# Performance work log

Measured on AMD Instinct MI355X. Metric: run time of the kernel, lower is better.

## Reference

```python
import jax, jax.numpy as jnp
import numpy as np

FEATURE_SIZE = 1000000  # padding index == FEATURE_SIZE
NEG_INF = -1e9


def _attn_pool(emb_table, hist_idx, ad_idx):
    # hist_idx: [B, L] int, ad_idx: [B] int
    hist = emb_table[hist_idx]          # [B, L, K] gather
    ad = emb_table[ad_idx]              # [B, K]
    score = jnp.einsum('blk,bk->bl', hist, ad)          # [B, L]
    score = jnp.where(hist_idx != FEATURE_SIZE, score, NEG_INF)
    w = jax.nn.softmax(score, axis=1)
    return jnp.einsum('blk,bl->bk', hist, w)            # [B, K]


def setup_inputs() -> dict:
    key = jax.random.key(0)
    ks = jax.random.split(key, 12)
    B, F, K = 4096, 8, 64
    V = FEATURE_SIZE + 1
    d_in = 3 * K + F * K  # 704
    inp = {
        'feature_idx': jax.random.randint(ks[0], (B, F), 0, FEATURE_SIZE),
        'hist_item': jax.random.randint(ks[1], (B, 350), 0, V),
        'hist_author': jax.random.randint(ks[2], (B, 250), 0, V),
        'hist_music': jax.random.randint(ks[3], (B, 100), 0, V),
        'emb_table': jax.random.normal(ks[4], (V, K), jnp.float32),
        'W1': jax.random.normal(ks[5], (d_in, 512), jnp.float32) * 0.02,
        'b1': jnp.zeros((512,), jnp.float32),
        'W2': jax.random.normal(ks[6], (512, 256), jnp.float32) * 0.02,
        'b2': jnp.zeros((256,), jnp.float32),
        'W3': jax.random.normal(ks[7], (256, 128), jnp.float32) * 0.02,
        'b3': jnp.zeros((128,), jnp.float32),
        'Wo': jax.random.normal(ks[8], (128, 1), jnp.float32) * 0.02,
        'bo': jnp.zeros((1,), jnp.float32),
    }
    return inp


def reference(feature_idx, hist_item, hist_author, hist_music, emb_table,
              W1, b1, W2, b2, W3, b3, Wo, bo):
    # ad indices for the three behavior features: columns 2, 3, 6
    pools = [
        _attn_pool(emb_table, hist_item, feature_idx[:, 2]),
        _attn_pool(emb_table, hist_author, feature_idx[:, 3]),
        _attn_pool(emb_table, hist_music, feature_idx[:, 6]),
    ]
    user_beha = jnp.concatenate(pools, axis=1)                    # [B, 3K]
    B = feature_idx.shape[0]
    ad_emb = emb_table[feature_idx].reshape(B, -1)                # [B, F*K]
    x = jnp.concatenate([user_beha, ad_emb], axis=1)              # [B, 704]
    x = jax.nn.relu(x @ W1 + b1)
    x = jax.nn.relu(x @ W2 + b2)
    x = jax.nn.relu(x @ W3 + b3)
    logits = x @ Wo + bo                                          # [B, 1]
    return logits
```

## Files before the change

### kernel.cpp

```cpp
#include <hip/hip_runtime.h>
#include <cstddef>

#define BATCH   4096
#define PAD_IDX 1000000
#define NEG_INF_F (-1e9f)

typedef __attribute__((ext_vector_type(8))) short bf16x8;
typedef __attribute__((ext_vector_type(4))) float f32x4;
typedef unsigned short u16;

__device__ __forceinline__ u16 f2bf(float f) {
    unsigned u = __float_as_uint(f);
    return (u16)((u + 0x7fffu + ((u >> 16) & 1u)) >> 16);
}
__device__ __forceinline__ float bf2f(u16 b) {
    return __uint_as_float(((unsigned)b) << 16);
}


#define UPD(s, v)                                     \
    {                                                 \
        float nm = fmaxf(m, (s));                     \
        float sc = __expf(m - nm);                    \
        float e  = __expf((s) - nm);                  \
        d = fmaf(d, sc, e);                           \
        acc.x = fmaf(acc.x, sc, e * (v).x);           \
        acc.y = fmaf(acc.y, sc, e * (v).y);           \
        acc.z = fmaf(acc.z, sc, e * (v).z);           \
        acc.w = fmaf(acc.w, sc, e * (v).w);           \
        m = nm;                                       \
    }

#define MERGE(P)                                                  \
    {                                                             \
        float mo  = __shfl_xor(m, P);                             \
        float d_o = __shfl_xor(d, P);                             \
        float ax = __shfl_xor(acc.x, P);                          \
        float ay = __shfl_xor(acc.y, P);                          \
        float az = __shfl_xor(acc.z, P);                          \
        float aw = __shfl_xor(acc.w, P);                          \
        float nm = fmaxf(m, mo);                                  \
        float sA = __expf(m - nm), sB = __expf(mo - nm);          \
        d = d * sA + d_o * sB;                                    \
        acc.x = acc.x * sA + ax * sB;                             \
        acc.y = acc.y * sA + ay * sB;                             \
        acc.z = acc.z * sA + az * sB;                             \
        acc.w = acc.w * sA + aw * sB;                             \
        m = nm;                                                   \
    }

#define QRED(s)                       \
    s += __shfl_xor(s, 1);            \
    s += __shfl_xor(s, 2);            \
    s += __shfl_xor(s, 4);            \
    s += __shfl_xor(s, 8);

__global__ void __launch_bounds__(256) build_x_kernel(
    const int* __restrict__ fidx,
    const int* __restrict__ hist_item,
    const int* __restrict__ hist_author,
    const int* __restrict__ hist_music,
    const float* __restrict__ emb,
    u16* __restrict__ x)
{
    const int w    = (blockIdx.x * 256 + threadIdx.x) >> 6;
    const int lane = threadIdx.x & 63;
    const int t16  = lane & 15;
    const int q    = lane >> 4;

    if (w < 3 * BATCH) {
        const int h = w >> 12;
        const int b = w & (BATCH - 1);
        int L, col, off;
        const int* hrow;
        if (h == 0)      { L = 350; col = 2; off = 0;   hrow = hist_item   + (size_t)b * 350; }
        else if (h == 1) { L = 250; col = 3; off = 64;  hrow = hist_author + (size_t)b * 250; }
        else             { L = 100; col = 6; off = 128; hrow = hist_music  + (size_t)b * 100; }

        const int ad_idx = fidx[b * 8 + col];
        const float4 ad4 = *(const float4*)(emb + (size_t)ad_idx * 64 + 4 * t16);

        float m = NEG_INF_F, d = 0.f;
        float4 acc = make_float4(0.f, 0.f, 0.f, 0.f);

        int l = 0;
        for (; l + 8 <= L; l += 8) {
            const int i0 = hrow[l + q];
            const int i1 = hrow[l + 4 + q];
            const float4 v0 = *(const float4*)(emb + (size_t)i0 * 64 + 4 * t16);
            const float4 v1 = *(const float4*)(emb + (size_t)i1 * 64 + 4 * t16);
            float s0 = v0.x * ad4.x + v0.y * ad4.y + v0.z * ad4.z + v0.w * ad4.w;
            float s1 = v1.x * ad4.x + v1.y * ad4.y + v1.z * ad4.z + v1.w * ad4.w;
            QRED(s0)
            QRED(s1)
            if (i0 == PAD_IDX) s0 = NEG_INF_F;
            if (i1 == PAD_IDX) s1 = NEG_INF_F;
            UPD(s0, v0)
            UPD(s1, v1)
        }
        for (; l < L; l += 4) {
            const int li = l + q;
            const int i0 = (li < L) ? hrow[li] : PAD_IDX;
            const float4 v0 = *(const float4*)(emb + (size_t)i0 * 64 + 4 * t16);
            float s0 = v0.x * ad4.x + v0.y * ad4.y + v0.z * ad4.z + v0.w * ad4.w;
            QRED(s0)
            if (i0 == PAD_IDX) s0 = NEG_INF_F;
            UPD(s0, v0)
        }

        MERGE(16)
        MERGE(32)

        if (lane < 16) {
            const float inv = 1.f / d;
            uint2 p;
            p.x = (unsigned)f2bf(acc.x * inv) | ((unsigned)f2bf(acc.y * inv) << 16);
            p.y = (unsigned)f2bf(acc.z * inv) | ((unsigned)f2bf(acc.w * inv) << 16);
            *(uint2*)(x + (size_t)b * 704 + off + 4 * t16) = p;
        }
    } else {
        const int tt = w - 3 * BATCH;
        const int b  = tt >> 1;
        const int f  = ((tt & 1) << 2) + q;
        const int idx = fidx[b * 8 + f];
        const float4 v = *(const float4*)(emb + (size_t)idx * 64 + 4 * t16);
        uint2 p;
        p.x = (unsigned)f2bf(v.x) | ((unsigned)f2bf(v.y) << 16);
        p.y = (unsigned)f2bf(v.z) | ((unsigned)f2bf(v.w) << 16);
        *(uint2*)(x + (size_t)b * 704 + 192 + (size_t)f * 64 + 4 * t16) = p;
    }
}

__global__ void __launch_bounds__(256) convert_weights(
    const float* __restrict__ W1, const float* __restrict__ W2, const float* __restrict__ W3,
    u16* __restrict__ W1T, u16* __restrict__ W2T, u16* __restrict__ W3T)
{
    int i = blockIdx.x * 256 + threadIdx.x;
    if (i < 704 * 512) {
        const int n = i / 704, k = i - n * 704;
        W1T[i] = f2bf(W1[(size_t)k * 512 + n]);
        return;
    }
    i -= 704 * 512;
    if (i < 512 * 256) {
        const int n = i / 512, k = i - n * 512;
        W2T[i] = f2bf(W2[(size_t)k * 256 + n]);
        return;
    }
    i -= 512 * 256;
    if (i < 256 * 128) {
        const int n = i / 256, k = i - n * 256;
        W3T[i] = f2bf(W3[(size_t)k * 128 + n]);
    }
}

template <int BN, bool RELU>
__global__ void __launch_bounds__(256) gemm_mfma(
    const u16* __restrict__ A, const u16* __restrict__ BT,
    const float* __restrict__ bias, u16* __restrict__ C,
    int M, int N, int K)
{
    constexpr int NB = BN / 16;
    __shared__ u16 As[64][40];
    __shared__ u16 Bs[BN][40];

    const int tid  = threadIdx.x;
    const int wave = tid >> 6, lane = tid & 63;
    const int quad = lane >> 4, l16 = lane & 15;
    const int bm = blockIdx.y * 64, bn = blockIdx.x * BN;

    const int srow = tid >> 2;
    const int sk   = (tid & 3) * 8;

    f32x4 acc[NB];
#pragma unroll
    for (int i = 0; i < NB; ++i) acc[i] = (f32x4){0.f, 0.f, 0.f, 0.f};

    const size_t a_base = (size_t)(bm + srow) * K + sk;

    for (int k0 = 0; k0 < K; k0 += 32) {
        *(float4*)&As[srow][sk] = *(const float4*)(A + a_base + k0);
#pragma unroll
        for (int r0 = 0; r0 < BN; r0 += 64) {
            *(float4*)&Bs[r0 + srow][sk] =
                *(const float4*)(BT + (size_t)(bn + r0 + srow) * K + k0 + sk);
        }
        __syncthreads();

        const bf16x8 af = *(const bf16x8*)&As[wave * 16 + l16][quad * 8];
#pragma unroll
        for (int ni = 0; ni < NB; ++ni) {
            const bf16x8 bf = *(const bf16x8*)&Bs[ni * 16 + l16][quad * 8];
            acc[ni] = __builtin_amdgcn_mfma_f32_16x16x32_bf16(af, bf, acc[ni], 0, 0, 0);
        }
        __syncthreads();
    }

#pragma unroll
    for (int ni = 0; ni < NB; ++ni) {
        const int col = bn + ni * 16 + l16;
        const float bv = bias[col];
#pragma unroll
        for (int r = 0; r < 4; ++r) {
            const int row = bm + wave * 16 + quad * 4 + r;
            float v = acc[ni][r] + bv;
            if (RELU) v = fmaxf(v, 0.f);
            C[(size_t)row * N + col] = f2bf(v);
        }
    }
}

__global__ void __launch_bounds__(256) out_layer(
    const u16* __restrict__ h3,
    const float* __restrict__ Wo,
    const float* __restrict__ bo,
    float* __restrict__ out, int M)
{
    const int w    = (blockIdx.x * 256 + threadIdx.x) >> 6;
    const int lane = threadIdx.x & 63;
    if (w >= M) return;
    float v = bf2f(h3[(size_t)w * 128 + lane]) * Wo[lane]
            + bf2f(h3[(size_t)w * 128 + 64 + lane]) * Wo[64 + lane];
    v += __shfl_xor(v, 32);
    v += __shfl_xor(v, 16);
    v += __shfl_xor(v, 8);
    v += __shfl_xor(v, 4);
    v += __shfl_xor(v, 2);
    v += __shfl_xor(v, 1);
    if (lane == 0) out[w] = v + bo[0];
}

extern "C" void kernel_launch(void* const* d_in, const int* in_sizes, int n_in,
                              void* d_out, int out_size, void* d_ws, size_t ws_size,
                              hipStream_t stream) {
    const int*   fidx  = (const int*)d_in[0];
    const int*   hitem = (const int*)d_in[1];
    const int*   hauth = (const int*)d_in[2];
    const int*   hmus  = (const int*)d_in[3];
    const float* emb   = (const float*)d_in[4];
    const float* W1 = (const float*)d_in[5];
    const float* b1 = (const float*)d_in[6];
    const float* W2 = (const float*)d_in[7];
    const float* b2 = (const float*)d_in[8];
    const float* W3 = (const float*)d_in[9];
    const float* b3 = (const float*)d_in[10];
    const float* Wo = (const float*)d_in[11];
    const float* bo = (const float*)d_in[12];
    float* out = (float*)d_out;

    u16* x   = (u16*)d_ws;
    u16* h1  = x   + (size_t)BATCH * 704;
    u16* h2  = h1  + (size_t)BATCH * 512;
    u16* h3  = h2  + (size_t)BATCH * 256;
    u16* w1t = h3  + (size_t)BATCH * 128;
    u16* w2t = w1t + (size_t)704 * 512;
    u16* w3t = w2t + (size_t)512 * 256;

    convert_weights<<<(704 * 512 + 512 * 256 + 256 * 128) / 256, 256, 0, stream>>>(
        W1, W2, W3, w1t, w2t, w3t);

    build_x_kernel<<<5 * BATCH / 4, 256, 0, stream>>>(fidx, hitem, hauth, hmus, emb, x);

    gemm_mfma<128, true><<<dim3(512 / 128, BATCH / 64), 256, 0, stream>>>(
        x, w1t, b1, h1, BATCH, 512, 704);
    gemm_mfma<64, true><<<dim3(256 / 64, BATCH / 64), 256, 0, stream>>>(
        h1, w2t, b2, h2, BATCH, 256, 512);
    gemm_mfma<64, true><<<dim3(128 / 64, BATCH / 64), 256, 0, stream>>>(
        h2, w3t, b3, h3, BATCH, 128, 256);

    out_layer<<<BATCH / 4, 256, 0, stream>>>(h3, Wo, bo, out, BATCH);
}
```

Measured before the change: 450.4 us.

## Fuse weight conversion into gather kernel, fuse last GEMM with output layer

Merges the weight transpose and bf16 conversion into the embedding gather/attention kernel as extra blocks, and switches the transpose to a shared-memory tiled version for coalesced reads and writes. The attention loop now prefetches indices one step ahead, loads four embedding rows per iteration, and keeps two independent online-softmax accumulators that are merged at the end, to expose more memory-level parallelism. The third GEMM is fused with the final output projection so h3 is never written to memory, and GEMM1 uses a narrower N tile to launch more blocks. This removes two kernel launches and some global traffic, at the cost of higher register pressure in the gather kernel.

```diff
diff --git a/kernel.cpp b/kernel.cpp
--- a/kernel.cpp
+++ b/kernel.cpp
@@ -17,18 +17,17 @@
     return __uint_as_float(((unsigned)b) << 16);
 }
 
-
-#define UPD(s, v)                                     \
-    {                                                 \
-        float nm = fmaxf(m, (s));                     \
-        float sc = __expf(m - nm);                    \
-        float e  = __expf((s) - nm);                  \
-        d = fmaf(d, sc, e);                           \
-        acc.x = fmaf(acc.x, sc, e * (v).x);           \
-        acc.y = fmaf(acc.y, sc, e * (v).y);           \
-        acc.z = fmaf(acc.z, sc, e * (v).z);           \
-        acc.w = fmaf(acc.w, sc, e * (v).w);           \
-        m = nm;                                       \
+#define UPD(mm, dd, aa, s, v)                          \
+    {                                                  \
+        float nm = fmaxf(mm, (s));                     \
+        float sc = __expf(mm - nm);                    \
+        float e  = __expf((s) - nm);                   \
+        dd = fmaf(dd, sc, e);                          \
+        aa.x = fmaf(aa.x, sc, e * (v).x);              \
+        aa.y = fmaf(aa.y, sc, e * (v).y);              \
+        aa.z = fmaf(aa.z, sc, e * (v).z);              \
+        aa.w = fmaf(aa.w, sc, e * (v).w);              \
+        mm = nm;                                       \
     }
 
 #define MERGE(P)                                                  \
@@ -55,106 +54,135 @@
     s += __shfl_xor(s, 4);            \
     s += __shfl_xor(s, 8);
 
-__global__ void __launch_bounds__(256) build_x_kernel(
+#define DOT4(v, a) ((v).x * (a).x + (v).y * (a).y + (v).z * (a).z + (v).w * (a).w)
+
+__global__ void __launch_bounds__(256) prep_kernel(
     const int* __restrict__ fidx,
     const int* __restrict__ hist_item,
     const int* __restrict__ hist_author,
     const int* __restrict__ hist_music,
     const float* __restrict__ emb,
-    u16* __restrict__ x)
+    const float* __restrict__ W1, const float* __restrict__ W2, const float* __restrict__ W3,
+    u16* __restrict__ x,
+    u16* __restrict__ w1t, u16* __restrict__ w2t, u16* __restrict__ w3t)
 {
-    const int w    = (blockIdx.x * 256 + threadIdx.x) >> 6;
-    const int lane = threadIdx.x & 63;
-    const int t16  = lane & 15;
-    const int q    = lane >> 4;
-
-    if (w < 3 * BATCH) {
-        const int h = w >> 12;
-        const int b = w & (BATCH - 1);
-        int L, col, off;
-        const int* hrow;
-        if (h == 0)      { L = 350; col = 2; off = 0;   hrow = hist_item   + (size_t)b * 350; }
-        else if (h == 1) { L = 250; col = 3; off = 64;  hrow = hist_author + (size_t)b * 250; }
-        else             { L = 100; col = 6; off = 128; hrow = hist_music  + (size_t)b * 100; }
-
-        const int ad_idx = fidx[b * 8 + col];
-        const float4 ad4 = *(const float4*)(emb + (size_t)ad_idx * 64 + 4 * t16);
-
-        float m = NEG_INF_F, d = 0.f;
-        float4 acc = make_float4(0.f, 0.f, 0.f, 0.f);
-
-        int l = 0;
-        for (; l + 8 <= L; l += 8) {
-            const int i0 = hrow[l + q];
-            const int i1 = hrow[l + 4 + q];
-            const float4 v0 = *(const float4*)(emb + (size_t)i0 * 64 + 4 * t16);
-            const float4 v1 = *(const float4*)(emb + (size_t)i1 * 64 + 4 * t16);
-            float s0 = v0.x * ad4.x + v0.y * ad4.y + v0.z * ad4.z + v0.w * ad4.w;
-            float s1 = v1.x * ad4.x + v1.y * ad4.y + v1.z * ad4.z + v1.w * ad4.w;
-            QRED(s0)
-            QRED(s1)
-            if (i0 == PAD_IDX) s0 = NEG_INF_F;
-            if (i1 == PAD_IDX) s1 = NEG_INF_F;
-            UPD(s0, v0)
-            UPD(s1, v1)
-        }
-        for (; l < L; l += 4) {
-            const int li = l + q;
-            const int i0 = (li < L) ? hrow[li] : PAD_IDX;
-            const float4 v0 = *(const float4*)(emb + (size_t)i0 * 64 + 4 * t16);
-            float s0 = v0.x * ad4.x + v0.y * ad4.y + v0.z * ad4.z + v0.w * ad4.w;
-            QRED(s0)
-            if (i0 == PAD_IDX) s0 = NEG_INF_F;
-            UPD(s0, v0)
-        }
-
-        MERGE(16)
-        MERGE(32)
-
-        if (lane < 16) {
-            const float inv = 1.f / d;
+    __shared__ float tile[32][33];
+    const int blk = blockIdx.x;
+
+    if (blk < 5120) {
+        const int w    = blk * 4 + (threadIdx.x >> 6);
+        const int lane = threadIdx.x & 63;
+        const int t16  = lane & 15;
+        const int q    = lane >> 4;
+
+        if (w < 3 * BATCH) {
+            const int h = w >> 12;
+            const int b = w & (BATCH - 1);
+            int L, col, off;
+            const int* hrow;
+            if (h == 0)      { L = 350; col = 2; off = 0;   hrow = hist_item   + (size_t)b * 350; }
+            else if (h == 1) { L = 250; col = 3; off = 64;  hrow = hist_author + (size_t)b * 250; }
+            else             { L = 100; col = 6; off = 128; hrow = hist_music  + (size_t)b * 100; }
+
+            const int ad_idx = fidx[b * 8 + col];
+            const float4 ad4 = *(const float4*)(emb + (size_t)ad_idx * 64 + 4 * t16);
+
+            float m = NEG_INF_F, d = 0.f;
+            float4 acc = make_float4(0.f, 0.f, 0.f, 0.f);
+            float mB = NEG_INF_F, dB = 0.f;
+            float4 aB = make_float4(0.f, 0.f, 0.f, 0.f);
+
+            int l = 0;
+            if (L >= 16) {
+                int n0 = hrow[q], n1 = hrow[4 + q], n2 = hrow[8 + q], n3 = hrow[12 + q];
+                while (true) {
+                    const int i0 = n0, i1 = n1, i2 = n2, i3 = n3;
+                    const float4 v0 = *(const float4*)(emb + (size_t)i0 * 64 + 4 * t16);
+                    const float4 v1 = *(const float4*)(emb + (size_t)i1 * 64 + 4 * t16);
+                    const float4 v2 = *(const float4*)(emb + (size_t)i2 * 64 + 4 * t16);
+                    const float4 v3 = *(const float4*)(emb + (size_t)i3 * 64 + 4 * t16);
+                    l += 16;
+                    const bool more = (l + 16 <= L);
+                    if (more) {
+                        n0 = hrow[l + q];      n1 = hrow[l + 4 + q];
+                        n2 = hrow[l + 8 + q];  n3 = hrow[l + 12 + q];
+                    }
+                    float s0 = DOT4(v0, ad4);
+                    float s1 = DOT4(v1, ad4);
+                    float s2 = DOT4(v2, ad4);
+                    float s3 = DOT4(v3, ad4);
+                    QRED(s0) QRED(s1) QRED(s2) QRED(s3)
+                    if (i0 == PAD_IDX) s0 = NEG_INF_F;
+                    if (i1 == PAD_IDX) s1 = NEG_INF_F;
+                    if (i2 == PAD_IDX) s2 = NEG_INF_F;
+                    if (i3 == PAD_IDX) s3 = NEG_INF_F;
+                    UPD(m, d, acc, s0, v0)
+                    UPD(mB, dB, aB, s1, v1)
+                    UPD(m, d, acc, s2, v2)
+                    UPD(mB, dB, aB, s3, v3)
+                    if (!more) break;
+                }
+            }
+            for (; l < L; l += 4) {
+                const int li = l + q;
+                const int i0 = (li < L) ? hrow[li] : PAD_IDX;
+                const float4 v0 = *(const float4*)(emb + (size_t)i0 * 64 + 4 * t16);
+                float s0 = DOT4(v0, ad4);
+                QRED(s0)
+                if (i0 == PAD_IDX) s0 = NEG_INF_F;
+                UPD(m, d, acc, s0, v0)
+            }
+
+            {
+                float nm = fmaxf(m, mB);
+                float eA = __expf(m - nm), eB = __expf(mB - nm);
+                d = d * eA + dB * eB;
+                acc.x = acc.x * eA + aB.x * eB;
+                acc.y = acc.y * eA + aB.y * eB;
+                acc.z = acc.z * eA + aB.z * eB;
+                acc.w = acc.w * eA + aB.w * eB;
+                m = nm;
+            }
+            MERGE(16)
+            MERGE(32)
+
+            if (lane < 16) {
+                const float inv = 1.f / d;
+                uint2 p;
+                p.x = (unsigned)f2bf(acc.x * inv) | ((unsigned)f2bf(acc.y * inv) << 16);
+                p.y = (unsigned)f2bf(acc.z * inv) | ((unsigned)f2bf(acc.w * inv) << 16);
+                *(uint2*)(x + (size_t)b * 704 + off + 4 * t16) = p;
+            }
+        } else {
+            const int tt = w - 3 * BATCH;
+            const int b  = tt >> 1;
+            const int f  = ((tt & 1) << 2) + q;
+            const int idx = fidx[b * 8 + f];
+            const float4 v = *(const float4*)(emb + (size_t)idx * 64 + 4 * t16);
             uint2 p;
-            p.x = (unsigned)f2bf(acc.x * inv) | ((unsigned)f2bf(acc.y * inv) << 16);
-            p.y = (unsigned)f2bf(acc.z * inv) | ((unsigned)f2bf(acc.w * inv) << 16);
-            *(uint2*)(x + (size_t)b * 704 + off + 4 * t16) = p;
+            p.x = (unsigned)f2bf(v.x) | ((unsigned)f2bf(v.y) << 16);
+            p.y = (unsigned)f2bf(v.z) | ((unsigned)f2bf(v.w) << 16);
+            *(uint2*)(x + (size_t)b * 704 + 192 + (size_t)f * 64 + 4 * t16) = p;
         }
     } else {
-        const int tt = w - 3 * BATCH;
-        const int b  = tt >> 1;
-        const int f  = ((tt & 1) << 2) + q;
-        const int idx = fidx[b * 8 + f];
-        const float4 v = *(const float4*)(emb + (size_t)idx * 64 + 4 * t16);
-        uint2 p;
-        p.x = (unsigned)f2bf(v.x) | ((unsigned)f2bf(v.y) << 16);
-        p.y = (unsigned)f2bf(v.z) | ((unsigned)f2bf(v.w) << 16);
-        *(uint2*)(x + (size_t)b * 704 + 192 + (size_t)f * 64 + 4 * t16) = p;
-    }
-}
-
-__global__ void __launch_bounds__(256) convert_weights(
-    const float* __restrict__ W1, const float* __restrict__ W2, const float* __restrict__ W3,
-    u16* __restrict__ W1T, u16* __restrict__ W2T, u16* __restrict__ W3T)
-{
-    int i = blockIdx.x * 256 + threadIdx.x;
-    if (i < 704 * 512) {
-        const int n = i / 704, k = i - n * 704;
-        W1T[i] = f2bf(W1[(size_t)k * 512 + n]);
-        return;
-    }
-    i -= 704 * 512;
-    if (i < 512 * 256) {
-        const int n = i / 512, k = i - n * 512;
-        W2T[i] = f2bf(W2[(size_t)k * 256 + n]);
-        return;
-    }
-    i -= 512 * 256;
-    if (i < 256 * 128) {
-        const int n = i / 256, k = i - n * 256;
-        W3T[i] = f2bf(W3[(size_t)k * 128 + n]);
-    }
-}
-
-template <int BN, bool RELU>
+        int t = blk - 5120;
+        const float* W; u16* WT; int K, N, tk, tn;
+        if (t < 352)      { W = W1; WT = w1t; K = 704; N = 512; tk = t % 22; tn = t / 22; }
+        else if (t < 480) { t -= 352; W = W2; WT = w2t; K = 512; N = 256; tk = t % 16; tn = t / 16; }
+        else              { t -= 480; W = W3; WT = w3t; K = 256; N = 128; tk = t % 8;  tn = t / 8;  }
+        const int k0 = tk * 32, n0 = tn * 32;
+        const int tx = threadIdx.x & 31, ty = threadIdx.x >> 5;
+#pragma unroll
+        for (int j = 0; j < 4; ++j)
+            tile[ty + 8 * j][tx] = W[(size_t)(k0 + ty + 8 * j) * N + n0 + tx];
+        __syncthreads();
+#pragma unroll
+        for (int j = 0; j < 4; ++j)
+            WT[(size_t)(n0 + ty + 8 * j) * K + k0 + tx] = f2bf(tile[tx][ty + 8 * j]);
+    }
+}
+
+template <int BN>
 __global__ void __launch_bounds__(256) gemm_mfma(
     const u16* __restrict__ A, const u16* __restrict__ BT,
     const float* __restrict__ bias, u16* __restrict__ C,
@@ -203,31 +231,77 @@
 #pragma unroll
         for (int r = 0; r < 4; ++r) {
             const int row = bm + wave * 16 + quad * 4 + r;
-            float v = acc[ni][r] + bv;
-            if (RELU) v = fmaxf(v, 0.f);
+            float v = fmaxf(acc[ni][r] + bv, 0.f);
             C[(size_t)row * N + col] = f2bf(v);
         }
     }
 }
 
-__global__ void __launch_bounds__(256) out_layer(
-    const u16* __restrict__ h3,
-    const float* __restrict__ Wo,
-    const float* __restrict__ bo,
-    float* __restrict__ out, int M)
+__global__ void __launch_bounds__(256) gemm3_out(
+    const u16* __restrict__ A, const u16* __restrict__ BT,
+    const float* __restrict__ bias,
+    const float* __restrict__ Wo, const float* __restrict__ bo,
+    float* __restrict__ out)
 {
-    const int w    = (blockIdx.x * 256 + threadIdx.x) >> 6;
-    const int lane = threadIdx.x & 63;
-    if (w >= M) return;
-    float v = bf2f(h3[(size_t)w * 128 + lane]) * Wo[lane]
-            + bf2f(h3[(size_t)w * 128 + 64 + lane]) * Wo[64 + lane];
-    v += __shfl_xor(v, 32);
-    v += __shfl_xor(v, 16);
-    v += __shfl_xor(v, 8);
-    v += __shfl_xor(v, 4);
-    v += __shfl_xor(v, 2);
-    v += __shfl_xor(v, 1);
-    if (lane == 0) out[w] = v + bo[0];
+    constexpr int K = 256, NB = 8;
+    __shared__ u16 As[64][40];
+    __shared__ u16 Bs[128][40];
+
+    const int tid  = threadIdx.x;
+    const int wave = tid >> 6, lane = tid & 63;
+    const int quad = lane >> 4, l16 = lane & 15;
+    const int bm = blockIdx.x * 64;
+
+    const int srow = tid >> 2;
+    const int sk   = (tid & 3) * 8;
+
+    f32x4 acc[NB];
+#pragma unroll
+    for (int i = 0; i < NB; ++i) acc[i] = (f32x4){0.f, 0.f, 0.f, 0.f};
+
+    const size_t a_base = (size_t)(bm + srow) * K + sk;
+
+    for (int k0 = 0; k0 < K; k0 += 32) {
+        *(float4*)&As[srow][sk] = *(const float4*)(A + a_base + k0);
+#pragma unroll
+        for (int r0 = 0; r0 < 128; r0 += 64) {
+            *(float4*)&Bs[r0 + srow][sk] =
+                *(const float4*)(BT + (size_t)(r0 + srow) * K + k0 + sk);
+        }
+        __syncthreads();
+
+        const bf16x8 af = *(const bf16x8*)&As[wave * 16 + l16][quad * 8];
+#pragma unroll
+        for (int ni = 0; ni < NB; ++ni) {
+            const bf16x8 bf = *(const bf16x8*)&Bs[ni * 16 + l16][quad * 8];
+            acc[ni] = __builtin_amdgcn_mfma_f32_16x16x32_bf16(af, bf, acc[ni], 0, 0, 0);
+        }
+        __syncthreads();
+    }
+
+    float part[4] = {0.f, 0.f, 0.f, 0.f};
+#pragma unroll
+    for (int ni = 0; ni < NB; ++ni) {
+        const int col = ni * 16 + l16;
+        const float bv = bias[col];
+        const float wv = Wo[col];
+#pragma unroll
+        for (int r = 0; r < 4; ++r)
+            part[r] = fmaf(fmaxf(acc[ni][r] + bv, 0.f), wv, part[r]);
+    }
+#pragma unroll
+    for (int r = 0; r < 4; ++r) {
+        part[r] += __shfl_xor(part[r], 1);
+        part[r] += __shfl_xor(part[r], 2);
+        part[r] += __shfl_xor(part[r], 4);
+        part[r] += __shfl_xor(part[r], 8);
+    }
+    if (l16 == 0) {
+        const float b0 = bo[0];
+#pragma unroll
+        for (int r = 0; r < 4; ++r)
+            out[bm + wave * 16 + quad * 4 + r] = part[r] + b0;
+    }
 }
 
 extern "C" void kernel_launch(void* const* d_in, const int* in_sizes, int n_in,
@@ -251,22 +325,16 @@
     u16* x   = (u16*)d_ws;
     u16* h1  = x   + (size_t)BATCH * 704;
     u16* h2  = h1  + (size_t)BATCH * 512;
-    u16* h3  = h2  + (size_t)BATCH * 256;
-    u16* w1t = h3  + (size_t)BATCH * 128;
+    u16* w1t = h2  + (size_t)BATCH * 256;
     u16* w2t = w1t + (size_t)704 * 512;
     u16* w3t = w2t + (size_t)512 * 256;
 
-    convert_weights<<<(704 * 512 + 512 * 256 + 256 * 128) / 256, 256, 0, stream>>>(
-        W1, W2, W3, w1t, w2t, w3t);
-
-    build_x_kernel<<<5 * BATCH / 4, 256, 0, stream>>>(fidx, hitem, hauth, hmus, emb, x);
-
-    gemm_mfma<128, true><<<dim3(512 / 128, BATCH / 64), 256, 0, stream>>>(
+    prep_kernel<<<5632, 256, 0, stream>>>(fidx, hitem, hauth, hmus, emb,
+                                          W1, W2, W3, x, w1t, w2t, w3t);
+
+    gemm_mfma<64><<<dim3(512 / 64, BATCH / 64), 256, 0, stream>>>(
         x, w1t, b1, h1, BATCH, 512, 704);
-    gemm_mfma<64, true><<<dim3(256 / 64, BATCH / 64), 256, 0, stream>>>(
+    gemm_mfma<64><<<dim3(256 / 64, BATCH / 64), 256, 0, stream>>>(
         h1, w2t, b2, h2, BATCH, 256, 512);
-    gemm_mfma<64, true><<<dim3(128 / 64, BATCH / 64), 256, 0, stream>>>(
-        h2, w3t, b3, h3, BATCH, 128, 256);
-
-    out_layer<<<BATCH / 4, 256, 0, stream>>>(h3, Wo, bo, out, BATCH);
-}
+    gemm3_out<<<BATCH / 64, 256, 0, stream>>>(h2, w3t, b3, Wo, bo, out);
+}
```

After: 445.3 us. Within noise of the previous version (-1.1%).
